# Optimization experiments

Measured on AMD Instinct MI355X. Metric: run time of the kernel, lower is better.

Reference implementation:

```python
import jax, jax.numpy as jnp
import numpy as np

SAMPLERATE = 22050
N_OCTAVES = 16
N_SAMPLES = 32768
MIN_FREQ = 20.0 / (SAMPLERATE // 2)
MAX_FREQ = 3000.0 / (SAMPLERATE // 2)
FREQ_RANGE = MAX_FREQ - MIN_FREQ
BASE_RESONANCE = 0.01


def max_norm(x, axis=-1, eps=1e-8):
    return x / (jnp.max(jnp.abs(x), axis=axis, keepdims=True) + eps)


def exponential_decay(decay_values, n_octaves):
    # decay_values: (B, E, 1). Note the original applies sigmoid here on top of
    # the sigmoid already applied in forward (sigmoid_decay=True) -> double sigmoid.
    dv = jax.nn.sigmoid(decay_values)  # (B, E, 1)
    resonance_factor = (1.0 - BASE_RESONANCE) * 0.99
    decay = BASE_RESONANCE + dv * resonance_factor  # (B, E, 1)
    logd = jnp.log(decay + 1e-12)
    b, e, _ = decay_values.shape
    # cumsum of a per-(b,e) constant over octaves, then exp (matches torch code;
    # F.interpolate to size==n_octaves is the identity here)
    logd = jnp.broadcast_to(logd, (b, e, n_octaves))
    return jnp.exp(jnp.cumsum(logd, axis=-1))  # (B, E, O)


def setup_inputs() -> dict:
    key = jax.random.key(0)
    k1, k2, k3 = jax.random.split(key, 3)
    B, E = 8, 64
    return {
        "f0": jax.random.uniform(k1, (B, E, 1), dtype=jnp.float32),
        "decay_coefficients": jax.random.normal(k2, (B, E, 1), dtype=jnp.float32),
        "unused": jnp.zeros((B, E, 1), dtype=jnp.float32),
        "freq_spacing": jax.random.uniform(k3, (B, E, 1), dtype=jnp.float32),
    }


def reference(f0, decay_coefficients, unused, freq_spacing):
    b, e, _ = f0.shape
    O, S = N_OCTAVES, N_SAMPLES

    f0 = jnp.abs(f0)  # (B, E, 1)
    # sigmoid_decay=True path: sigmoid applied before exponential_decay
    exp_decays = exponential_decay(jax.nn.sigmoid(decay_coefficients), O)  # (B, E, O)

    f0 = (MIN_FREQ + f0 * FREQ_RANGE) * jnp.pi  # (B, E, 1)

    # freq_spacing repeated over octaves then cumsum -> per-octave factors
    factors = jnp.cumsum(jnp.broadcast_to(freq_spacing, (b, e, O)), axis=-1)
    f0s = f0 * factors  # (B, E, O)

    # nyquist cutoff
    f0s = f0s * (f0s < 1.0)

    # phase: cumsum over samples of constant per-octave frequency (faithful to torch)
    phase = jnp.cumsum(jnp.broadcast_to(f0s[..., None], (b, e, O, S)), axis=-1)
    osc = jnp.sin(phase)  # (B, E, O, S)

    osc = osc * exp_decays[..., None]
    osc = jnp.sum(osc, axis=2)  # (B, E, S)
    return max_norm(osc, axis=-1)
```

## Files before the change

kernel.cpp:

```cpp
#include <hip/hip_runtime.h>
#include <math.h>

#define N_OCT 16
#define NPAIR 8
#define NS    32768
#define TPB   512
#define SPT   (NS / TPB)
#define N_BE  512

typedef float v2f __attribute__((ext_vector_type(2)));

static __device__ __forceinline__ v2f fma2(v2f a, v2f b, v2f c) {
    return __builtin_elementwise_fma(a, b, c);
}

__global__ __launch_bounds__(TPB, 1)
void f0res_kernel(const float* __restrict__ f0_in,
                  const float* __restrict__ dc_in,
                  const float* __restrict__ fs_in,
                  float* __restrict__ out)
{
    __shared__ double sR[N_OCT];
    __shared__ float  sCH[N_OCT], sCL[N_OCT], sAMP[N_OCT];
    __shared__ float  wmax[TPB / 64];

    const int be = blockIdx.x;
    const int t  = threadIdx.x;

    if (t < N_OCT) {
        const int o = t;
        const float f0a = fabsf(f0_in[be]);
        const float dc  = dc_in[be];
        const float fs  = fs_in[be];

        const float MINF = (float)(20.0 / 11025.0);
        const float FRNG = (float)(3000.0 / 11025.0 - 20.0 / 11025.0);

        const float s1    = 1.0f / (1.0f + __expf(-dc));
        const float dv    = 1.0f / (1.0f + __expf(-s1));
        const float decay = 0.01f + dv * 0.9801f;
        const float logd  = __logf(decay + 1e-12f);
        const float f0r   = (MINF + f0a * FRNG) * 3.14159274101257324f;

        float cl = 0.f, cf = 0.f;
        for (int i = 0; i <= o; ++i) { cl += logd; cf += fs; }
        float ed  = __expf(cl);
        float f0s = f0r * cf;
        float a   = ed;
        if (!(f0s < 1.0f)) { a = 0.0f; f0s = 0.0f; }

        const double inv2pi = 0.15915494309189535;
        double r = (double)f0s * inv2pi;

        double drev = r * (double)TPB;
        drev -= floor(drev);
        double c2d = 2.0 * cos(drev * 6.283185307179586);
        float  ch  = (float)c2d;

        sR[o]   = r;
        sCH[o]  = ch;
        sCL[o]  = (float)(c2d - (double)ch);
        sAMP[o] = a;
    }
    __syncthreads();

    v2f xp[NPAIR], xc[NPAIR], c2h[NPAIR], c2l[NPAIR], sx[NPAIR], sp[NPAIR];

    #pragma unroll
    for (int o = 0; o < N_OCT; ++o) {
        const double r = sR[o];
        const float  a = sAMP[o];

        double p0 = r * (double)(t + 1);
        p0 -= floor(p0);
        double pm = r * (double)(t + 1 - TPB);
        pm -= floor(pm);
        float xcur  = a * __builtin_amdgcn_sinf((float)p0);
        float xprev = a * __builtin_amdgcn_sinf((float)pm);

        const int j = o >> 1;
        if ((o & 1) == 0) {
            xc[j].x = xcur;   xp[j].x = xprev;
            c2h[j].x = sCH[o]; c2l[j].x = sCL[o];
        } else {
            xc[j].y = xcur;   xp[j].y = xprev;
            c2h[j].y = sCH[o]; c2l[j].y = sCL[o];
        }
    }
    #pragma unroll
    for (int j = 0; j < NPAIR; ++j) { sx[j] = xc[j]; sp[j] = xp[j]; }

    float lmax = 0.0f;
    #pragma unroll 4
    for (int k = 0; k < SPT; ++k) {
        v2f acc2 = (v2f)(0.0f);
        #pragma unroll
        for (int j = 0; j < NPAIR; ++j) {
            acc2 += xc[j];
            v2f xn = fma2(c2h[j], xc[j], fma2(c2l[j], xc[j], -xp[j]));
            xp[j] = xc[j];
            xc[j] = xn;
        }
        lmax = fmaxf(lmax, fabsf(acc2.x + acc2.y));
    }

    #pragma unroll
    for (int off = 32; off > 0; off >>= 1)
        lmax = fmaxf(lmax, __shfl_down(lmax, off, 64));
    if ((t & 63) == 0) wmax[t >> 6] = lmax;
    __syncthreads();
    float bmax = wmax[0];
    #pragma unroll
    for (int w = 1; w < TPB / 64; ++w) bmax = fmaxf(bmax, wmax[w]);

    const float norm = 1.0f / (bmax + 1e-8f);

    #pragma unroll
    for (int j = 0; j < NPAIR; ++j) {
        xc[j] = sx[j] * norm;
        xp[j] = sp[j] * norm;
    }

    float* __restrict__ orow = out + (size_t)be * NS;
    #pragma unroll 4
    for (int k = 0; k < SPT; ++k) {
        v2f acc2 = (v2f)(0.0f);
        #pragma unroll
        for (int j = 0; j < NPAIR; ++j) {
            acc2 += xc[j];
            v2f xn = fma2(c2h[j], xc[j], fma2(c2l[j], xc[j], -xp[j]));
            xp[j] = xc[j];
            xc[j] = xn;
        }
        orow[k * TPB + t] = acc2.x + acc2.y;
    }
}

extern "C" void kernel_launch(void* const* d_in, const int* in_sizes, int n_in,
                              void* d_out, int out_size, void* d_ws, size_t ws_size,
                              hipStream_t stream) {
    const float* f0 = (const float*)d_in[0];
    const float* dc = (const float*)d_in[1];
    const float* fs = (const float*)d_in[3];
    float* out = (float*)d_out;
    (void)d_ws; (void)ws_size;

    hipLaunchKernelGGL(f0res_kernel, dim3(N_BE), dim3(TPB),
                       0, stream, f0, dc, fs, out);
}
```

Baseline: 109.4 us.

## Skip dead octaves via ballot count and templated body; run second pass backward

Counts octaves below Nyquist with a wavefront ballot and dispatches to a templated body that only carries the live octave pairs, so the cutoff octaves (which have zero amplitude and are monotone in cumulative spacing) no longer cost recurrence FMAs. The normalized output pass now runs the recurrence backward from the end state of the max pass, so the saved initial states are no longer kept in registers. The block size doubles to 1024 threads, which halves samples per thread. The risks are code-size growth from eight instantiations, drift from running the recurrence in reverse, and reliance on live octaves being a prefix.

```diff
diff --git a/kernel.cpp b/kernel.cpp
--- a/kernel.cpp
+++ b/kernel.cpp
@@ -2,9 +2,8 @@
 #include <math.h>
 
 #define N_OCT 16
-#define NPAIR 8
 #define NS    32768
-#define TPB   512
+#define TPB   1024
 #define SPT   (NS / TPB)
 #define N_BE  512
 
@@ -12,6 +11,79 @@
 
 static __device__ __forceinline__ v2f fma2(v2f a, v2f b, v2f c) {
     return __builtin_elementwise_fma(a, b, c);
+}
+
+template<int NP>
+static __device__ __forceinline__ void run_body(
+    const int t,
+    const double* __restrict__ sR, const float* __restrict__ sCH,
+    const float* __restrict__ sCL, const float* __restrict__ sAMP,
+    float* __restrict__ wmax, float* __restrict__ orow)
+{
+    v2f xp[NP], xc[NP], c2h[NP], c2l[NP];
+
+    #pragma unroll
+    for (int o = 0; o < 2 * NP; ++o) {
+        const double r = sR[o];
+        const float  a = sAMP[o];
+        double p0 = r * (double)(t + 1);
+        p0 -= floor(p0);
+        double pm = r * (double)(t + 1 - TPB);
+        pm -= floor(pm);
+        float xcur  = a * __builtin_amdgcn_sinf((float)p0);
+        float xprev = a * __builtin_amdgcn_sinf((float)pm);
+        const int j = o >> 1;
+        if ((o & 1) == 0) {
+            xc[j].x = xcur;   xp[j].x = xprev;
+            c2h[j].x = sCH[o]; c2l[j].x = sCL[o];
+        } else {
+            xc[j].y = xcur;   xp[j].y = xprev;
+            c2h[j].y = sCH[o]; c2l[j].y = sCL[o];
+        }
+    }
+
+    float lmax = 0.0f;
+    #pragma unroll 4
+    for (int k = 0; k < SPT; ++k) {
+        v2f acc2 = (v2f)(0.0f);
+        #pragma unroll
+        for (int j = 0; j < NP; ++j) {
+            acc2 += xc[j];
+            v2f xn = fma2(c2h[j], xc[j], fma2(c2l[j], xc[j], -xp[j]));
+            xp[j] = xc[j];
+            xc[j] = xn;
+        }
+        lmax = fmaxf(lmax, fabsf(acc2.x + acc2.y));
+    }
+
+    #pragma unroll
+    for (int off = 32; off > 0; off >>= 1)
+        lmax = fmaxf(lmax, __shfl_down(lmax, off, 64));
+    if ((t & 63) == 0) wmax[t >> 6] = lmax;
+    __syncthreads();
+    float bmax = wmax[0];
+    #pragma unroll
+    for (int w = 1; w < TPB / 64; ++w) bmax = fmaxf(bmax, wmax[w]);
+    const float norm = 1.0f / (bmax + 1e-8f);
+
+    v2f cur[NP], nxt[NP];
+    #pragma unroll
+    for (int j = 0; j < NP; ++j) {
+        cur[j] = xp[j] * norm;
+        nxt[j] = xc[j] * norm;
+    }
+    #pragma unroll 4
+    for (int m = SPT - 1; m >= 0; --m) {
+        v2f acc2 = (v2f)(0.0f);
+        #pragma unroll
+        for (int j = 0; j < NP; ++j) {
+            acc2 += cur[j];
+            v2f pv = fma2(c2h[j], cur[j], fma2(c2l[j], cur[j], -nxt[j]));
+            nxt[j] = cur[j];
+            cur[j] = pv;
+        }
+        orow[m * TPB + t] = acc2.x + acc2.y;
+    }
 }
 
 __global__ __launch_bounds__(TPB, 1)
@@ -23,6 +95,7 @@
     __shared__ double sR[N_OCT];
     __shared__ float  sCH[N_OCT], sCL[N_OCT], sAMP[N_OCT];
     __shared__ float  wmax[TPB / 64];
+    __shared__ int    sLive;
 
     const int be = blockIdx.x;
     const int t  = threadIdx.x;
@@ -47,7 +120,11 @@
         float ed  = __expf(cl);
         float f0s = f0r * cf;
         float a   = ed;
-        if (!(f0s < 1.0f)) { a = 0.0f; f0s = 0.0f; }
+        const bool live = (f0s < 1.0f);
+        if (!live) { a = 0.0f; f0s = 0.0f; }
+
+        unsigned long long lm = __ballot(live);
+        if (o == 0) sLive = __popcll(lm);
 
         const double inv2pi = 0.15915494309189535;
         double r = (double)f0s * inv2pi;
@@ -64,75 +141,23 @@
     }
     __syncthreads();
 
-    v2f xp[NPAIR], xc[NPAIR], c2h[NPAIR], c2l[NPAIR], sx[NPAIR], sp[NPAIR];
+    const int NP = (sLive + 1) >> 1;
+    float* __restrict__ orow = out + (size_t)be * NS;
 
-    #pragma unroll
-    for (int o = 0; o < N_OCT; ++o) {
-        const double r = sR[o];
-        const float  a = sAMP[o];
-
-        double p0 = r * (double)(t + 1);
-        p0 -= floor(p0);
-        double pm = r * (double)(t + 1 - TPB);
-        pm -= floor(pm);
-        float xcur  = a * __builtin_amdgcn_sinf((float)p0);
-        float xprev = a * __builtin_amdgcn_sinf((float)pm);
-
-        const int j = o >> 1;
-        if ((o & 1) == 0) {
-            xc[j].x = xcur;   xp[j].x = xprev;
-            c2h[j].x = sCH[o]; c2l[j].x = sCL[o];
-        } else {
-            xc[j].y = xcur;   xp[j].y = xprev;
-            c2h[j].y = sCH[o]; c2l[j].y = sCL[o];
-        }
+    switch (NP) {
+    case 0: {
+        #pragma unroll
+        for (int m = 0; m < SPT; ++m) orow[m * TPB + t] = 0.0f;
+        break;
     }
-    #pragma unroll
-    for (int j = 0; j < NPAIR; ++j) { sx[j] = xc[j]; sp[j] = xp[j]; }
-
-    float lmax = 0.0f;
-    #pragma unroll 4
-    for (int k = 0; k < SPT; ++k) {
-        v2f acc2 = (v2f)(0.0f);
-        #pragma unroll
-        for (int j = 0; j < NPAIR; ++j) {
-            acc2 += xc[j];
-            v2f xn = fma2(c2h[j], xc[j], fma2(c2l[j], xc[j], -xp[j]));
-            xp[j] = xc[j];
-            xc[j] = xn;
-        }
-        lmax = fmaxf(lmax, fabsf(acc2.x + acc2.y));
-    }
-
-    #pragma unroll
-    for (int off = 32; off > 0; off >>= 1)
-        lmax = fmaxf(lmax, __shfl_down(lmax, off, 64));
-    if ((t & 63) == 0) wmax[t >> 6] = lmax;
-    __syncthreads();
-    float bmax = wmax[0];
-    #pragma unroll
-    for (int w = 1; w < TPB / 64; ++w) bmax = fmaxf(bmax, wmax[w]);
-
-    const float norm = 1.0f / (bmax + 1e-8f);
-
-    #pragma unroll
-    for (int j = 0; j < NPAIR; ++j) {
-        xc[j] = sx[j] * norm;
-        xp[j] = sp[j] * norm;
-    }
-
-    float* __restrict__ orow = out + (size_t)be * NS;
-    #pragma unroll 4
-    for (int k = 0; k < SPT; ++k) {
-        v2f acc2 = (v2f)(0.0f);
-        #pragma unroll
-        for (int j = 0; j < NPAIR; ++j) {
-            acc2 += xc[j];
-            v2f xn = fma2(c2h[j], xc[j], fma2(c2l[j], xc[j], -xp[j]));
-            xp[j] = xc[j];
-            xc[j] = xn;
-        }
-        orow[k * TPB + t] = acc2.x + acc2.y;
+    case 1: run_body<1>(t, sR, sCH, sCL, sAMP, wmax, orow); break;
+    case 2: run_body<2>(t, sR, sCH, sCL, sAMP, wmax, orow); break;
+    case 3: run_body<3>(t, sR, sCH, sCL, sAMP, wmax, orow); break;
+    case 4: run_body<4>(t, sR, sCH, sCL, sAMP, wmax, orow); break;
+    case 5: run_body<5>(t, sR, sCH, sCL, sAMP, wmax, orow); break;
+    case 6: run_body<6>(t, sR, sCH, sCL, sAMP, wmax, orow); break;
+    case 7: run_body<7>(t, sR, sCH, sCL, sAMP, wmax, orow); break;
+    default: run_body<8>(t, sR, sCH, sCL, sAMP, wmax, orow); break;
     }
 }
 
```

Result: no change. 108.7 us (-0.6%).

## Split synthesis into stage and normalize kernels with fp16 staging and live-octave skipping

Applied to the files above, without the earlier changes.

The old single kernel ran the oscillator recurrence twice: once to find the row max and once to write normalized output. It now runs once, stores unnormalized sums in fp16 to workspace and records a per-chunk max. A second kernel reads the staged values, reduces the four chunk maxima and writes the scaled float output. Each row is split over four blocks of 256 threads. The recurrence length is chosen from the count of octaves below the Nyquist cutoff so dead octaves are skipped, and initial phases use 32-bit fixed-point arithmetic instead of doubles. In exchange it adds extra memory traffic for the staging buffer, a second launch, and fp16 rounding of the output before normalization.

```diff
diff --git a/kernel.cpp b/kernel.cpp
--- a/kernel.cpp
+++ b/kernel.cpp
@@ -1,32 +1,34 @@
 #include <hip/hip_runtime.h>
 #include <math.h>
 
-#define N_OCT 16
-#define NPAIR 8
-#define NS    32768
-#define TPB   512
-#define SPT   (NS / TPB)
-#define N_BE  512
+#define N_OCT  16
+#define NS     32768
+#define TPB    256
+#define NSPLIT 4
+#define CHUNK  (NS / NSPLIT)
+#define SPT    (CHUNK / TPB)
+#define N_BE   512
+#define NBLK   (N_BE * NSPLIT)
 
 typedef float v2f __attribute__((ext_vector_type(2)));
+typedef _Float16 h4 __attribute__((ext_vector_type(4)));
 
 static __device__ __forceinline__ v2f fma2(v2f a, v2f b, v2f c) {
     return __builtin_elementwise_fma(a, b, c);
 }
 
-__global__ __launch_bounds__(TPB, 1)
-void f0res_kernel(const float* __restrict__ f0_in,
-                  const float* __restrict__ dc_in,
-                  const float* __restrict__ fs_in,
-                  float* __restrict__ out)
-{
-    __shared__ double sR[N_OCT];
-    __shared__ float  sCH[N_OCT], sCL[N_OCT], sAMP[N_OCT];
-    __shared__ float  wmax[TPB / 64];
-
-    const int be = blockIdx.x;
-    const int t  = threadIdx.x;
-
+#define WS_STAGE(ws) ((_Float16*)(ws))
+#define WS_MAX(ws)   ((float*)((char*)(ws) + (size_t)N_BE * NS * 2))
+
+
+static __device__ __forceinline__ void make_consts(
+    int be, int t,
+    const float* __restrict__ f0_in, const float* __restrict__ dc_in,
+    const float* __restrict__ fs_in,
+    unsigned int* __restrict__ sRQ,
+    float* __restrict__ sCH, float* __restrict__ sCL,
+    float* __restrict__ sAMP, int* __restrict__ sLive)
+{
     if (t < N_OCT) {
         const int o = t;
         const float f0a = fabsf(f0_in[be]);
@@ -47,61 +49,113 @@
         float ed  = __expf(cl);
         float f0s = f0r * cf;
         float a   = ed;
-        if (!(f0s < 1.0f)) { a = 0.0f; f0s = 0.0f; }
+        const bool live = (f0s < 1.0f);
+        if (!live) { a = 0.0f; f0s = 0.0f; }
+
+        unsigned long long lm = __ballot(live);
+        if (o == 0) *sLive = __popcll(lm);
 
         const double inv2pi = 0.15915494309189535;
-        double r = (double)f0s * inv2pi;
+        const double r = (double)f0s * inv2pi;
+        const unsigned int rq = (unsigned int)llrint(r * 4294967296.0);
 
         double drev = r * (double)TPB;
         drev -= floor(drev);
         double c2d = 2.0 * cos(drev * 6.283185307179586);
         float  ch  = (float)c2d;
 
-        sR[o]   = r;
+        sRQ[o]  = rq;
         sCH[o]  = ch;
         sCL[o]  = (float)(c2d - (double)ch);
         sAMP[o] = a;
     }
-    __syncthreads();
-
-    v2f xp[NPAIR], xc[NPAIR], c2h[NPAIR], c2l[NPAIR], sx[NPAIR], sp[NPAIR];
-
+}
+
+static __device__ __forceinline__ float q32_phase(int n, unsigned int rq)
+{
+    const unsigned int frac = (unsigned int)n * rq;
+    return (float)frac * 2.3283064365386963e-10f;
+}
+
+template<int NP>
+static __device__ __forceinline__ float body_stage(
+    int base, int t,
+    const unsigned int* __restrict__ sRQ,
+    const float* __restrict__ sCH, const float* __restrict__ sCL,
+    const float* __restrict__ sAMP,
+    _Float16* __restrict__ stage)
+{
+    v2f xp[NP], xc[NP], c2h[NP], c2l[NP];
+
+    const int n1 = base + t + 1;
+    const int n0 = base + t + 1 - TPB;
     #pragma unroll
-    for (int o = 0; o < N_OCT; ++o) {
-        const double r = sR[o];
-        const float  a = sAMP[o];
-
-        double p0 = r * (double)(t + 1);
-        p0 -= floor(p0);
-        double pm = r * (double)(t + 1 - TPB);
-        pm -= floor(pm);
-        float xcur  = a * __builtin_amdgcn_sinf((float)p0);
-        float xprev = a * __builtin_amdgcn_sinf((float)pm);
-
+    for (int o = 0; o < 2 * NP; ++o) {
+        const unsigned int rq = sRQ[o];
+        const float a = sAMP[o];
+        float xcur  = a * __builtin_amdgcn_sinf(q32_phase(n1, rq));
+        float xprev = a * __builtin_amdgcn_sinf(q32_phase(n0, rq));
         const int j = o >> 1;
         if ((o & 1) == 0) {
-            xc[j].x = xcur;   xp[j].x = xprev;
+            xc[j].x = xcur;    xp[j].x = xprev;
             c2h[j].x = sCH[o]; c2l[j].x = sCL[o];
         } else {
-            xc[j].y = xcur;   xp[j].y = xprev;
+            xc[j].y = xcur;    xp[j].y = xprev;
             c2h[j].y = sCH[o]; c2l[j].y = sCL[o];
         }
     }
-    #pragma unroll
-    for (int j = 0; j < NPAIR; ++j) { sx[j] = xc[j]; sp[j] = xp[j]; }
 
     float lmax = 0.0f;
     #pragma unroll 4
     for (int k = 0; k < SPT; ++k) {
         v2f acc2 = (v2f)(0.0f);
         #pragma unroll
-        for (int j = 0; j < NPAIR; ++j) {
+        for (int j = 0; j < NP; ++j) {
             acc2 += xc[j];
             v2f xn = fma2(c2h[j], xc[j], fma2(c2l[j], xc[j], -xp[j]));
             xp[j] = xc[j];
             xc[j] = xn;
         }
-        lmax = fmaxf(lmax, fabsf(acc2.x + acc2.y));
+        const float acc = acc2.x + acc2.y;
+        stage[k * TPB + t] = (_Float16)acc;
+        lmax = fmaxf(lmax, fabsf(acc));
+    }
+    return lmax;
+}
+
+__global__ __launch_bounds__(TPB)
+void f0res_stage_k(const float* __restrict__ f0_in,
+                   const float* __restrict__ dc_in,
+                   const float* __restrict__ fs_in,
+                   void* __restrict__ ws)
+{
+    __shared__ unsigned int sRQ[N_OCT];
+    __shared__ float sCH[N_OCT], sCL[N_OCT], sAMP[N_OCT];
+    __shared__ float wmax[TPB / 64];
+    __shared__ int   sLive;
+
+    const int bid = blockIdx.x;
+    const int be  = bid >> 2;
+    const int q   = bid & 3;
+    const int t   = threadIdx.x;
+    const int base = q * CHUNK;
+
+    make_consts(be, t, f0_in, dc_in, fs_in, sRQ, sCH, sCL, sAMP, &sLive);
+    __syncthreads();
+
+    const int L  = sLive;
+    _Float16* __restrict__ stage = WS_STAGE(ws) + (size_t)be * NS + base;
+
+    float lmax = 0.0f;
+    if (L == 0) {
+        #pragma unroll
+        for (int k = 0; k < SPT; ++k) stage[k * TPB + t] = (_Float16)0.0f;
+    } else if (L <= 4) {
+        lmax = body_stage<2>(base, t, sRQ, sCH, sCL, sAMP, stage);
+    } else if (L <= 8) {
+        lmax = body_stage<4>(base, t, sRQ, sCH, sCL, sAMP, stage);
+    } else {
+        lmax = body_stage<8>(base, t, sRQ, sCH, sCL, sAMP, stage);
     }
 
     #pragma unroll
@@ -109,30 +163,39 @@
         lmax = fmaxf(lmax, __shfl_down(lmax, off, 64));
     if ((t & 63) == 0) wmax[t >> 6] = lmax;
     __syncthreads();
-    float bmax = wmax[0];
+    if (t == 0) {
+        float bmax = wmax[0];
+        #pragma unroll
+        for (int w = 1; w < TPB / 64; ++w) bmax = fmaxf(bmax, wmax[w]);
+        WS_MAX(ws)[bid] = bmax;
+    }
+}
+
+__global__ __launch_bounds__(TPB)
+void f0res_norm_k(const void* __restrict__ ws,
+                  float* __restrict__ out)
+{
+    const int bid = blockIdx.x;
+    const int be  = bid >> 2;
+    const int q   = bid & 3;
+    const int t   = threadIdx.x;
+
+    const float* mx = WS_MAX(ws) + (be << 2);
+    const float bmax = fmaxf(fmaxf(mx[0], mx[1]), fmaxf(mx[2], mx[3]));
+    const float norm = 1.0f / (bmax + 1e-8f);
+
+    const h4* __restrict__ src =
+        (const h4*)(WS_STAGE(ws) + (size_t)be * NS + q * CHUNK);
+    float4* __restrict__ dst = (float4*)(out + (size_t)be * NS + q * CHUNK);
+
     #pragma unroll
-    for (int w = 1; w < TPB / 64; ++w) bmax = fmaxf(bmax, wmax[w]);
-
-    const float norm = 1.0f / (bmax + 1e-8f);
-
-    #pragma unroll
-    for (int j = 0; j < NPAIR; ++j) {
-        xc[j] = sx[j] * norm;
-        xp[j] = sp[j] * norm;
-    }
-
-    float* __restrict__ orow = out + (size_t)be * NS;
-    #pragma unroll 4
-    for (int k = 0; k < SPT; ++k) {
-        v2f acc2 = (v2f)(0.0f);
-        #pragma unroll
-        for (int j = 0; j < NPAIR; ++j) {
-            acc2 += xc[j];
-            v2f xn = fma2(c2h[j], xc[j], fma2(c2l[j], xc[j], -xp[j]));
-            xp[j] = xc[j];
-            xc[j] = xn;
-        }
-        orow[k * TPB + t] = acc2.x + acc2.y;
+    for (int i = 0; i < CHUNK / 4 / TPB; ++i) {
+        const int idx = i * TPB + t;
+        h4 v = src[idx];
+        float4 o;
+        o.x = (float)v.x * norm; o.y = (float)v.y * norm;
+        o.z = (float)v.z * norm; o.w = (float)v.w * norm;
+        dst[idx] = o;
     }
 }
 
@@ -143,8 +206,9 @@
     const float* dc = (const float*)d_in[1];
     const float* fs = (const float*)d_in[3];
     float* out = (float*)d_out;
-    (void)d_ws; (void)ws_size;
-
-    hipLaunchKernelGGL(f0res_kernel, dim3(N_BE), dim3(TPB),
-                       0, stream, f0, dc, fs, out);
-}
+
+    hipLaunchKernelGGL(f0res_stage_k, dim3(NBLK), dim3(TPB), 0, stream,
+                       f0, dc, fs, d_ws);
+    hipLaunchKernelGGL(f0res_norm_k, dim3(NBLK), dim3(TPB), 0, stream,
+                       d_ws, out);
+}
```

Result: slower. 112.9 us (+3.2%).
